# Optimization experiments

Hardware: AMD Instinct MI355X
Metric: run time of the kernel (lower is better)

Reference implementation:

```python
import jax, jax.numpy as jnp
import numpy as np
import math

D_MODEL = 1024
NUM_HEADS = 16
ROPE_THETA = 10000.0
BATCH = 4
SEQ = 2048


def apply_rope(x, pos, theta=ROPE_THETA):
    # x: (b, h, s, d_k), pos: (s,) int positions
    d = x.shape[-1]
    inv_freq = theta ** (-jnp.arange(0, d, 2, dtype=jnp.float32) / d)  # (d/2,)
    ang = pos.astype(jnp.float32)[:, None] * inv_freq                  # (s, d/2)
    cos, sin = jnp.cos(ang), jnp.sin(ang)
    x1, x2 = x[..., 0::2], x[..., 1::2]
    # interleave rotated pairs back to last dim
    out = jnp.stack([x1 * cos - x2 * sin, x1 * sin + x2 * cos], axis=-1)
    return out.reshape(x.shape)


def setup_inputs() -> dict:
    key = jax.random.key(0)
    ks = jax.random.split(key, 5)
    scale = 1.0 / math.sqrt(D_MODEL)
    return {
        "x": jax.random.normal(ks[0], (BATCH, SEQ, D_MODEL), dtype=jnp.float32),
        "token_positions": jnp.arange(SEQ, dtype=jnp.int64 if jax.config.jax_enable_x64 else jnp.int32),
        "Wq": jax.random.normal(ks[1], (D_MODEL, D_MODEL), dtype=jnp.float32) * scale,
        "Wk": jax.random.normal(ks[2], (D_MODEL, D_MODEL), dtype=jnp.float32) * scale,
        "Wv": jax.random.normal(ks[3], (D_MODEL, D_MODEL), dtype=jnp.float32) * scale,
        "Wo": jax.random.normal(ks[4], (D_MODEL, D_MODEL), dtype=jnp.float32) * scale,
    }


def reference(x, token_positions, Wq, Wk, Wv, Wo):
    b, s, d_model = x.shape
    h = NUM_HEADS
    d_k = d_model // h

    def proj_split(W):
        # Linear: y = x @ W.T (W is (out,in)); then split heads -> (b, h, s, d_k)
        y = jnp.einsum('bsi,oi->bso', x, W)
        return y.reshape(b, s, h, d_k).transpose(0, 2, 1, 3)

    q = apply_rope(proj_split(Wq), token_positions)
    k = apply_rope(proj_split(Wk), token_positions)
    v = proj_split(Wv)

    scores = jnp.einsum('bhqd,bhkd->bhqk', q, k) / jnp.asarray(math.sqrt(d_k), x.dtype)
    causal = jnp.tril(jnp.ones((s, s), dtype=bool))  # (s, s) keep lower triangle
    scores = jnp.where(causal, scores, jnp.asarray(-jnp.inf, scores.dtype))
    attn = jax.nn.softmax(scores, axis=-1)
    out = jnp.einsum('bhqk,bhkd->bhqd', attn, v)
    out = out.transpose(0, 2, 1, 3).reshape(b, s, d_model)
    return jnp.einsum('bsi,oi->bso', out, Wo)
```

## Files before the change

kernel.cpp:

```cpp
#include <hip/hip_runtime.h>
#include <cstdint>
#include <cstddef>


typedef __attribute__((ext_vector_type(8))) short bf16x8;
typedef __attribute__((ext_vector_type(4))) float f32x4;

#define LOG2E 1.4426950408889634f

__device__ __forceinline__ unsigned short f2bf(float f) {
  unsigned int u = __builtin_bit_cast(unsigned int, f);
  unsigned int r = (u + 0x7FFFu + ((u >> 16) & 1u)) >> 16;
  return (unsigned short)r;
}
__device__ __forceinline__ float bf2f(unsigned short h) {
  return __builtin_bit_cast(float, (unsigned int)h << 16);
}
__device__ __forceinline__ unsigned int packbf2(float a, float b) {
  return (unsigned int)f2bf(a) | ((unsigned int)f2bf(b) << 16);
}
__device__ __forceinline__ int swz(int idx) {
  return idx ^ (((idx >> 6) & 7) << 3);
}

__global__ __launch_bounds__(256) void cvt_kernel(const float* __restrict__ in,
                                                  unsigned short* __restrict__ out,
                                                  int n8) {
  int i = blockIdx.x * 256 + threadIdx.x;
  if (i < n8) {
    float4 u0 = ((const float4*)in)[i * 2];
    float4 u1 = ((const float4*)in)[i * 2 + 1];
    uint4 v = {packbf2(u0.x, u0.y), packbf2(u0.z, u0.w),
               packbf2(u1.x, u1.y), packbf2(u1.z, u1.w)};
    ((uint4*)out)[i] = v;
  }
}
__global__ __launch_bounds__(256) void cvt_w3(const float* __restrict__ w0,
                                              const float* __restrict__ w1,
                                              const float* __restrict__ w2,
                                              unsigned short* __restrict__ dst) {
  const float* src = blockIdx.y == 0 ? w0 : (blockIdx.y == 1 ? w1 : w2);
  unsigned short* d = dst + (size_t)blockIdx.y * 1024 * 1024;
  int i = blockIdx.x * 256 + threadIdx.x;
  float4 u0 = ((const float4*)src)[i * 2];
  float4 u1 = ((const float4*)src)[i * 2 + 1];
  uint4 v = {packbf2(u0.x, u0.y), packbf2(u0.z, u0.w),
             packbf2(u1.x, u1.y), packbf2(u1.z, u1.w)};
  ((uint4*)d)[i] = v;
}

__global__ __launch_bounds__(256) void gemm_qkv(const unsigned short* __restrict__ Xb,
                                                const unsigned short* __restrict__ Wb3,
                                                unsigned short* __restrict__ Qb,
                                                unsigned short* __restrict__ Kb,
                                                unsigned short* __restrict__ Vtb) {
  __shared__ alignas(16) unsigned short As[128 * 64];
  __shared__ alignas(16) unsigned short Bs[128 * 64];
  const int t = threadIdx.x;
  const int lane = t & 63;
  const int w = t >> 6;
  const int wr = w >> 1, wc = w & 1;
  const int fr = lane & 15, fq = lane >> 4;
  const int m0 = blockIdx.x * 128;
  const int sel = blockIdx.y >> 3;
  const int n0 = (blockIdx.y & 7) * 128;
  const unsigned short* Wp = Wb3 + (size_t)sel * 1024 * 1024;
  const int K = 1024;

  const f32x4 zero = {0.f, 0.f, 0.f, 0.f};
  f32x4 acc[4][4];
#pragma unroll
  for (int m = 0; m < 4; ++m)
#pragma unroll
    for (int n = 0; n < 4; ++n) acc[m][n] = zero;

  for (int k0 = 0; k0 < K; k0 += 64) {
#pragma unroll
    for (int cc = 0; cc < 4; ++cc) {
      int c = w * 4 + cc;
      int flat = c * 512 + lane * 8;
      int row = flat >> 6, col = flat & 63;
      __builtin_amdgcn_global_load_lds(
          (const __attribute__((address_space(1))) void*)(Xb + (size_t)(m0 + row) * K + (k0 + col)),
          (__attribute__((address_space(3))) void*)&As[c * 512], 16, 0, 0);
      __builtin_amdgcn_global_load_lds(
          (const __attribute__((address_space(1))) void*)(Wp + (size_t)(n0 + row) * K + (k0 + col)),
          (__attribute__((address_space(3))) void*)&Bs[c * 512], 16, 0, 0);
    }
    __syncthreads();
#pragma unroll
    for (int kk = 0; kk < 2; ++kk) {
      bf16x8 a[4], b[4];
#pragma unroll
      for (int m = 0; m < 4; ++m)
        a[m] = *(const bf16x8*)&As[(wr * 64 + m * 16 + fr) * 64 + kk * 32 + fq * 8];
#pragma unroll
      for (int n = 0; n < 4; ++n)
        b[n] = *(const bf16x8*)&Bs[(wc * 64 + n * 16 + fr) * 64 + kk * 32 + fq * 8];
#pragma unroll
      for (int m = 0; m < 4; ++m)
#pragma unroll
        for (int n = 0; n < 4; ++n)
          acc[m][n] = __builtin_amdgcn_mfma_f32_16x16x32_bf16(a[m], b[n], acc[m][n], 0, 0, 0);
    }
    __syncthreads();
  }

#pragma unroll
  for (int m = 0; m < 4; ++m)
#pragma unroll
    for (int n = 0; n < 4; ++n) {
      int row = m0 + wr * 64 + m * 16 + fq * 4;
      int col = n0 + wc * 64 + n * 16 + fr;
      if (sel < 2) {
        unsigned short* Cp = sel ? Kb : Qb;
#pragma unroll
        for (int j = 0; j < 4; ++j)
          Cp[(size_t)(row + j) * 1024 + col] = f2bf(acc[m][n][j]);
      } else {
        int b = row >> 11, s = row & 2047;
        int h = col >> 6, d = col & 63;
        ushort4 v4 = {f2bf(acc[m][n][0]), f2bf(acc[m][n][1]),
                      f2bf(acc[m][n][2]), f2bf(acc[m][n][3])};
        *(ushort4*)&Vtb[(((size_t)b * 16 + h) * 64 + d) * 2048 + s] = v4;
      }
    }
}

__global__ __launch_bounds__(256) void rope_kernel(unsigned short* __restrict__ Q,
                                                   unsigned short* __restrict__ Kb,
                                                   const int* __restrict__ tp) {
  int idx = blockIdx.x * 256 + threadIdx.x;
  unsigned short* ptr = blockIdx.y ? Kb : Q;
  const float scale = blockIdx.y ? 1.0f : 0.125f * LOG2E;
  int flat8 = idx * 8;
  int r = flat8 >> 10;
  int colbase = flat8 & 1023;
  int ibase = (colbase & 63) >> 1;
  int s = r & 2047;
  float pos = (float)tp[s];
  const float cexp = -13.287712379549449f / 32.0f;

  uint4 v = *(const uint4*)&ptr[flat8];
  unsigned int* vp = (unsigned int*)&v;
  uint4 o;
  unsigned int* op = (unsigned int*)&o;
#pragma unroll
  for (int p = 0; p < 4; ++p) {
    float inv = exp2f((float)(ibase + p) * cexp);
    float ang = pos * inv;
    float sn, cs;
    sincosf(ang, &sn, &cs);
    float x1 = bf2f((unsigned short)(vp[p] & 0xFFFFu));
    float x2 = bf2f((unsigned short)(vp[p] >> 16));
    op[p] = packbf2((x1 * cs - x2 * sn) * scale, (x1 * sn + x2 * cs) * scale);
  }
  *(uint4*)&ptr[flat8] = o;
}

__global__ __launch_bounds__(512, 2) void attn_kernel(const unsigned short* __restrict__ Q,
                                                      const unsigned short* __restrict__ K,
                                                      const unsigned short* __restrict__ Vt_g,
                                                      unsigned short* __restrict__ O) {
  __shared__ alignas(16) unsigned short Ks[64 * 64];
  __shared__ alignas(16) unsigned short Vt[64 * 64];
  const int t = threadIdx.x;
  const int lane = t & 63, w = t >> 6;
  const int fr = lane & 15, fq = lane >> 4;
  const int gblk = (blockIdx.x & 7) * 64 + (blockIdx.x >> 3);
  const int qt = gblk & 7;
  const int hb = gblk >> 3;
  const int h = hb & 15, b = hb >> 4;
  const int q0 = qt * 256;
  const size_t base = ((size_t)b * 2048) * 1024 + (size_t)h * 64;
  const size_t vbase = ((size_t)b * 16 + h) * 64 * 2048;
  const f32x4 zero = {0.f, 0.f, 0.f, 0.f};

  bf16x8 qf[2][2];
#pragma unroll
  for (int g = 0; g < 2; ++g)
#pragma unroll
    for (int kk = 0; kk < 2; ++kk)
      qf[g][kk] = *(const bf16x8*)&Q[base + (size_t)(q0 + w * 32 + g * 16 + fr) * 1024 + kk * 32 + fq * 8];

  float m_[2] = {-INFINITY, -INFINITY};
  float l_[2] = {0.f, 0.f};
  f32x4 oaccT[2][4];
#pragma unroll
  for (int g = 0; g < 2; ++g)
#pragma unroll
    for (int n = 0; n < 4; ++n) oaccT[g][n] = zero;

  const int sflat = t * 8;
  const int srow = sflat >> 6, scol = sflat & 63;
  const int sdst = swz(sflat);
  uint4 kr = *(const uint4*)&K[base + (size_t)srow * 1024 + scol];
  uint4 vr = *(const uint4*)&Vt_g[vbase + (size_t)srow * 2048 + scol];
  const int kvend = q0 + 256;
  const int wq = q0 + w * 32;

  for (int kv0 = 0; kv0 < kvend; kv0 += 64) {
    __syncthreads();
    *(uint4*)&Ks[sdst] = kr;
    *(uint4*)&Vt[sdst] = vr;
    __syncthreads();
    if (kv0 + 64 < kvend) {
      kr = *(const uint4*)&K[base + (size_t)(kv0 + 64 + srow) * 1024 + scol];
      vr = *(const uint4*)&Vt_g[vbase + (size_t)srow * 2048 + kv0 + 64 + scol];
    }

    if (kv0 <= wq + 31) {
      bf16x8 kf[2][4];
#pragma unroll
      for (int kk = 0; kk < 2; ++kk)
#pragma unroll
        for (int n = 0; n < 4; ++n)
          kf[kk][n] = *(const bf16x8*)&Ks[swz((n * 16 + fr) * 64 + kk * 32 + fq * 8)];

#pragma unroll
      for (int g = 0; g < 2; ++g) {
        if (kv0 > wq + g * 16 + 15) continue;
        f32x4 sa[4];
#pragma unroll
        for (int n = 0; n < 4; ++n) sa[n] = zero;
#pragma unroll
        for (int kk = 0; kk < 2; ++kk)
#pragma unroll
          for (int n = 0; n < 4; ++n)
            sa[n] = __builtin_amdgcn_mfma_f32_16x16x32_bf16(kf[kk][n], qf[g][kk], sa[n], 0, 0, 0);

        const int dd = kv0 - wq - g * 16;
        const bool diag = (dd > -63);
        float pmax = -3.0e38f;
#pragma unroll
        for (int n = 0; n < 4; ++n)
#pragma unroll
          for (int j = 0; j < 4; ++j) {
            float s = sa[n][j];
            if (diag && (n * 16 + fq * 4 + j + dd > fr)) s = -3.0e38f;
            sa[n][j] = s;
            pmax = fmaxf(pmax, s);
          }
        pmax = fmaxf(pmax, __shfl_xor(pmax, 16));
        pmax = fmaxf(pmax, __shfl_xor(pmax, 32));
        float mn = fmaxf(m_[g], pmax);
        float alpha = exp2f(m_[g] - mn);
        m_[g] = mn;
        float ps = 0.f;
#pragma unroll
        for (int n = 0; n < 4; ++n)
#pragma unroll
          for (int j = 0; j < 4; ++j) {
            float e = exp2f(sa[n][j] - mn);
            sa[n][j] = e;
            ps += e;
          }
        ps += __shfl_xor(ps, 16);
        ps += __shfl_xor(ps, 32);
        l_[g] = l_[g] * alpha + ps;
#pragma unroll
        for (int n = 0; n < 4; ++n)
#pragma unroll
          for (int j = 0; j < 4; ++j) oaccT[g][n][j] *= alpha;

        unsigned R[4][2], F[4][2];
#pragma unroll
        for (int n = 0; n < 4; ++n)
#pragma unroll
          for (int pp = 0; pp < 2; ++pp)
            R[n][pp] = packbf2(sa[n][2 * pp], sa[n][2 * pp + 1]);
#pragma unroll
        for (int pp = 0; pp < 2; ++pp) {
          unsigned t0 = (fq < 2) ? R[1][pp] : R[0][pp];
          unsigned t1 = (fq < 2) ? R[3][pp] : R[2][pp];
          t0 = (unsigned)__shfl_xor((int)t0, 32);
          t1 = (unsigned)__shfl_xor((int)t1, 32);
          unsigned G0 = (fq < 2) ? R[0][pp] : t0;
          unsigned G1 = (fq < 2) ? t0 : R[1][pp];
          unsigned G2 = (fq < 2) ? R[2][pp] : t1;
          unsigned G3 = (fq < 2) ? t1 : R[3][pp];
          unsigned u0 = ((fq & 1) == 0) ? G1 : G0;
          unsigned u1 = ((fq & 1) == 0) ? G3 : G2;
          u0 = (unsigned)__shfl_xor((int)u0, 16);
          u1 = (unsigned)__shfl_xor((int)u1, 16);
          F[0][pp] = ((fq & 1) == 0) ? G0 : u0;
          F[1][pp] = ((fq & 1) == 0) ? u0 : G1;
          F[2][pp] = ((fq & 1) == 0) ? G2 : u1;
          F[3][pp] = ((fq & 1) == 0) ? u1 : G3;
        }
        union U8 { unsigned u[4]; bf16x8 v; };
        U8 pb0, pb1;
        pb0.u[0] = F[0][0]; pb0.u[1] = F[0][1]; pb0.u[2] = F[1][0]; pb0.u[3] = F[1][1];
        pb1.u[0] = F[2][0]; pb1.u[1] = F[2][1]; pb1.u[2] = F[3][0]; pb1.u[3] = F[3][1];

#pragma unroll
        for (int n = 0; n < 4; ++n) {
          bf16x8 vf0 = *(const bf16x8*)&Vt[swz((n * 16 + fr) * 64 + 0 * 32 + fq * 8)];
          oaccT[g][n] = __builtin_amdgcn_mfma_f32_16x16x32_bf16(vf0, pb0.v, oaccT[g][n], 0, 0, 0);
          bf16x8 vf1 = *(const bf16x8*)&Vt[swz((n * 16 + fr) * 64 + 1 * 32 + fq * 8)];
          oaccT[g][n] = __builtin_amdgcn_mfma_f32_16x16x32_bf16(vf1, pb1.v, oaccT[g][n], 0, 0, 0);
        }
      }
    }
  }

#pragma unroll
  for (int g = 0; g < 2; ++g) {
    float rl = 1.0f / l_[g];
#pragma unroll
    for (int n = 0; n < 4; ++n) {
      ushort4 v4 = {f2bf(oaccT[g][n][0] * rl), f2bf(oaccT[g][n][1] * rl),
                    f2bf(oaccT[g][n][2] * rl), f2bf(oaccT[g][n][3] * rl)};
      *(ushort4*)&O[base + (size_t)(q0 + w * 32 + g * 16 + fr) * 1024 + n * 16 + fq * 4] = v4;
    }
  }
}

__global__ __launch_bounds__(256) void gemm_out_bf(const unsigned short* __restrict__ Ap,
                                                   const unsigned short* __restrict__ Wp,
                                                   float* __restrict__ Cp) {
  __shared__ alignas(16) unsigned short As[128 * 64];
  __shared__ alignas(16) unsigned short Bs[128 * 64];
  const int t = threadIdx.x;
  const int lane = t & 63;
  const int w = t >> 6;
  const int wr = w >> 1, wc = w & 1;
  const int fr = lane & 15, fq = lane >> 4;
  const int m0 = blockIdx.x * 128, n0 = blockIdx.y * 128;
  const int K = 1024, N = 1024;

  const f32x4 zero = {0.f, 0.f, 0.f, 0.f};
  f32x4 acc[4][4];
#pragma unroll
  for (int m = 0; m < 4; ++m)
#pragma unroll
    for (int n = 0; n < 4; ++n) acc[m][n] = zero;

  for (int k0 = 0; k0 < K; k0 += 64) {
#pragma unroll
    for (int cc = 0; cc < 4; ++cc) {
      int c = w * 4 + cc;
      int flat = c * 512 + lane * 8;
      int row = flat >> 6, col = flat & 63;
      __builtin_amdgcn_global_load_lds(
          (const __attribute__((address_space(1))) void*)(Ap + (size_t)(m0 + row) * K + (k0 + col)),
          (__attribute__((address_space(3))) void*)&As[c * 512], 16, 0, 0);
      __builtin_amdgcn_global_load_lds(
          (const __attribute__((address_space(1))) void*)(Wp + (size_t)(n0 + row) * K + (k0 + col)),
          (__attribute__((address_space(3))) void*)&Bs[c * 512], 16, 0, 0);
    }
    __syncthreads();
#pragma unroll
    for (int kk = 0; kk < 2; ++kk) {
      bf16x8 a[4], b[4];
#pragma unroll
      for (int m = 0; m < 4; ++m)
        a[m] = *(const bf16x8*)&As[(wr * 64 + m * 16 + fr) * 64 + kk * 32 + fq * 8];
#pragma unroll
      for (int n = 0; n < 4; ++n)
        b[n] = *(const bf16x8*)&Bs[(wc * 64 + n * 16 + fr) * 64 + kk * 32 + fq * 8];
#pragma unroll
      for (int m = 0; m < 4; ++m)
#pragma unroll
        for (int n = 0; n < 4; ++n)
          acc[m][n] = __builtin_amdgcn_mfma_f32_16x16x32_bf16(a[m], b[n], acc[m][n], 0, 0, 0);
    }
    __syncthreads();
  }

#pragma unroll
  for (int m = 0; m < 4; ++m)
#pragma unroll
    for (int n = 0; n < 4; ++n) {
      int row = m0 + wr * 64 + m * 16 + fq * 4;
      int col = n0 + wc * 64 + n * 16 + fr;
#pragma unroll
      for (int j = 0; j < 4; ++j)
        Cp[(size_t)(row + j) * N + col] = acc[m][n][j];
    }
}

extern "C" void kernel_launch(void* const* d_in, const int* in_sizes, int n_in,
                              void* d_out, int out_size, void* d_ws, size_t ws_size,
                              hipStream_t stream) {
  const float* x  = (const float*)d_in[0];
  const int* tp   = (const int*)d_in[1];
  const float* Wq = (const float*)d_in[2];
  const float* Wk = (const float*)d_in[3];
  const float* Wv = (const float*)d_in[4];
  const float* Wo = (const float*)d_in[5];
  float* out = (float*)d_out;

  const size_t MAT = (size_t)8192 * 1024;
  unsigned short* Qb  = (unsigned short*)d_ws;
  unsigned short* Kb  = Qb + MAT;
  unsigned short* Vtb = Kb + MAT;
  unsigned short* Xb  = Vtb + MAT;
  unsigned short* Ob  = Xb;
  unsigned short* Wb3 = (unsigned short*)d_out;
  unsigned short* WoB = Qb;

  cvt_kernel<<<4096, 256, 0, stream>>>(x, Xb, 8192 * 1024 / 8);
  cvt_w3<<<dim3(512, 3), 256, 0, stream>>>(Wq, Wk, Wv, Wb3);
  gemm_qkv<<<dim3(64, 24), 256, 0, stream>>>(Xb, Wb3, Qb, Kb, Vtb);
  rope_kernel<<<dim3(4096, 2), 256, 0, stream>>>(Qb, Kb, tp);
  attn_kernel<<<512, 512, 0, stream>>>(Qb, Kb, Vtb, Ob);
  cvt_kernel<<<512, 256, 0, stream>>>(Wo, WoB, 1024 * 1024 / 8);
  gemm_out_bf<<<dim3(64, 8), 256, 0, stream>>>(Ob, WoB, out);
}
```

Measured before the change: 413.4 us.

## Balance causal attention work by pairing light and heavy query tiles per block

```diff
diff --git a/kernel.cpp b/kernel.cpp
--- a/kernel.cpp
+++ b/kernel.cpp
@@ -158,160 +158,177 @@
   *(uint4*)&ptr[flat8] = o;
 }
 
-__global__ __launch_bounds__(512, 2) void attn_kernel(const unsigned short* __restrict__ Q,
-                                                      const unsigned short* __restrict__ K,
-                                                      const unsigned short* __restrict__ Vt_g,
-                                                      unsigned short* __restrict__ O) {
+__global__ __launch_bounds__(256) void attn_kernel(const unsigned short* __restrict__ Q,
+                                                   const unsigned short* __restrict__ K,
+                                                   const unsigned short* __restrict__ Vt_g,
+                                                   unsigned short* __restrict__ O) {
   __shared__ alignas(16) unsigned short Ks[64 * 64];
   __shared__ alignas(16) unsigned short Vt[64 * 64];
   const int t = threadIdx.x;
   const int lane = t & 63, w = t >> 6;
   const int fr = lane & 15, fq = lane >> 4;
   const int gblk = (blockIdx.x & 7) * 64 + (blockIdx.x >> 3);
-  const int qt = gblk & 7;
+  const int pairidx = gblk & 7;
   const int hb = gblk >> 3;
   const int h = hb & 15, b = hb >> 4;
-  const int q0 = qt * 256;
   const size_t base = ((size_t)b * 2048) * 1024 + (size_t)h * 64;
   const size_t vbase = ((size_t)b * 16 + h) * 64 * 2048;
   const f32x4 zero = {0.f, 0.f, 0.f, 0.f};
 
-  bf16x8 qf[2][2];
-#pragma unroll
-  for (int g = 0; g < 2; ++g)
-#pragma unroll
-    for (int kk = 0; kk < 2; ++kk)
-      qf[g][kk] = *(const bf16x8*)&Q[base + (size_t)(q0 + w * 32 + g * 16 + fr) * 1024 + kk * 32 + fq * 8];
-
-  float m_[2] = {-INFINITY, -INFINITY};
-  float l_[2] = {0.f, 0.f};
-  f32x4 oaccT[2][4];
-#pragma unroll
-  for (int g = 0; g < 2; ++g)
-#pragma unroll
-    for (int n = 0; n < 4; ++n) oaccT[g][n] = zero;
-
   const int sflat = t * 8;
-  const int srow = sflat >> 6, scol = sflat & 63;
-  const int sdst = swz(sflat);
-  uint4 kr = *(const uint4*)&K[base + (size_t)srow * 1024 + scol];
-  uint4 vr = *(const uint4*)&Vt_g[vbase + (size_t)srow * 2048 + scol];
-  const int kvend = q0 + 256;
-  const int wq = q0 + w * 32;
-
-  for (int kv0 = 0; kv0 < kvend; kv0 += 64) {
-    __syncthreads();
-    *(uint4*)&Ks[sdst] = kr;
-    *(uint4*)&Vt[sdst] = vr;
-    __syncthreads();
-    if (kv0 + 64 < kvend) {
-      kr = *(const uint4*)&K[base + (size_t)(kv0 + 64 + srow) * 1024 + scol];
-      vr = *(const uint4*)&Vt_g[vbase + (size_t)srow * 2048 + kv0 + 64 + scol];
-    }
-
-    if (kv0 <= wq + 31) {
-      bf16x8 kf[2][4];
+  const int srow0 = sflat >> 6, scol = sflat & 63;
+
+  for (int pass = 0; pass < 2; ++pass) {
+    const int qt = pass ? (15 - pairidx) : pairidx;
+    const int q0 = qt * 128;
+    const int wq = q0 + w * 32;
+    const int kvend = q0 + 128;
+
+    bf16x8 qf[2][2];
+#pragma unroll
+    for (int g = 0; g < 2; ++g)
 #pragma unroll
       for (int kk = 0; kk < 2; ++kk)
-#pragma unroll
-        for (int n = 0; n < 4; ++n)
-          kf[kk][n] = *(const bf16x8*)&Ks[swz((n * 16 + fr) * 64 + kk * 32 + fq * 8)];
-
-#pragma unroll
-      for (int g = 0; g < 2; ++g) {
-        if (kv0 > wq + g * 16 + 15) continue;
-        f32x4 sa[4];
-#pragma unroll
-        for (int n = 0; n < 4; ++n) sa[n] = zero;
-#pragma unroll
-        for (int kk = 0; kk < 2; ++kk)
-#pragma unroll
-          for (int n = 0; n < 4; ++n)
-            sa[n] = __builtin_amdgcn_mfma_f32_16x16x32_bf16(kf[kk][n], qf[g][kk], sa[n], 0, 0, 0);
-
-        const int dd = kv0 - wq - g * 16;
-        const bool diag = (dd > -63);
-        float pmax = -3.0e38f;
-#pragma unroll
-        for (int n = 0; n < 4; ++n)
-#pragma unroll
-          for (int j = 0; j < 4; ++j) {
-            float s = sa[n][j];
-            if (diag && (n * 16 + fq * 4 + j + dd > fr)) s = -3.0e38f;
-            sa[n][j] = s;
-            pmax = fmaxf(pmax, s);
-          }
-        pmax = fmaxf(pmax, __shfl_xor(pmax, 16));
-        pmax = fmaxf(pmax, __shfl_xor(pmax, 32));
-        float mn = fmaxf(m_[g], pmax);
-        float alpha = exp2f(m_[g] - mn);
-        m_[g] = mn;
-        float ps = 0.f;
-#pragma unroll
-        for (int n = 0; n < 4; ++n)
-#pragma unroll
-          for (int j = 0; j < 4; ++j) {
-            float e = exp2f(sa[n][j] - mn);
-            sa[n][j] = e;
-            ps += e;
-          }
-        ps += __shfl_xor(ps, 16);
-        ps += __shfl_xor(ps, 32);
-        l_[g] = l_[g] * alpha + ps;
-#pragma unroll
-        for (int n = 0; n < 4; ++n)
-#pragma unroll
-          for (int j = 0; j < 4; ++j) oaccT[g][n][j] *= alpha;
-
-        unsigned R[4][2], F[4][2];
-#pragma unroll
-        for (int n = 0; n < 4; ++n)
-#pragma unroll
-          for (int pp = 0; pp < 2; ++pp)
-            R[n][pp] = packbf2(sa[n][2 * pp], sa[n][2 * pp + 1]);
-#pragma unroll
-        for (int pp = 0; pp < 2; ++pp) {
-          unsigned t0 = (fq < 2) ? R[1][pp] : R[0][pp];
-          unsigned t1 = (fq < 2) ? R[3][pp] : R[2][pp];
-          t0 = (unsigned)__shfl_xor((int)t0, 32);
-          t1 = (unsigned)__shfl_xor((int)t1, 32);
-          unsigned G0 = (fq < 2) ? R[0][pp] : t0;
-          unsigned G1 = (fq < 2) ? t0 : R[1][pp];
-          unsigned G2 = (fq < 2) ? R[2][pp] : t1;
-          unsigned G3 = (fq < 2) ? t1 : R[3][pp];
-          unsigned u0 = ((fq & 1) == 0) ? G1 : G0;
-          unsigned u1 = ((fq & 1) == 0) ? G3 : G2;
-          u0 = (unsigned)__shfl_xor((int)u0, 16);
-          u1 = (unsigned)__shfl_xor((int)u1, 16);
-          F[0][pp] = ((fq & 1) == 0) ? G0 : u0;
-          F[1][pp] = ((fq & 1) == 0) ? u0 : G1;
-          F[2][pp] = ((fq & 1) == 0) ? G2 : u1;
-          F[3][pp] = ((fq & 1) == 0) ? u1 : G3;
-        }
-        union U8 { unsigned u[4]; bf16x8 v; };
-        U8 pb0, pb1;
-        pb0.u[0] = F[0][0]; pb0.u[1] = F[0][1]; pb0.u[2] = F[1][0]; pb0.u[3] = F[1][1];
-        pb1.u[0] = F[2][0]; pb1.u[1] = F[2][1]; pb1.u[2] = F[3][0]; pb1.u[3] = F[3][1];
-
-#pragma unroll
-        for (int n = 0; n < 4; ++n) {
-          bf16x8 vf0 = *(const bf16x8*)&Vt[swz((n * 16 + fr) * 64 + 0 * 32 + fq * 8)];
-          oaccT[g][n] = __builtin_amdgcn_mfma_f32_16x16x32_bf16(vf0, pb0.v, oaccT[g][n], 0, 0, 0);
-          bf16x8 vf1 = *(const bf16x8*)&Vt[swz((n * 16 + fr) * 64 + 1 * 32 + fq * 8)];
-          oaccT[g][n] = __builtin_amdgcn_mfma_f32_16x16x32_bf16(vf1, pb1.v, oaccT[g][n], 0, 0, 0);
+        qf[g][kk] = *(const bf16x8*)&Q[base + (size_t)(q0 + w * 32 + g * 16 + fr) * 1024 + kk * 32 + fq * 8];
+
+    float m_[2] = {-INFINITY, -INFINITY};
+    float l_[2] = {0.f, 0.f};
+    f32x4 oaccT[2][4];
+#pragma unroll
+    for (int g = 0; g < 2; ++g)
+#pragma unroll
+      for (int n = 0; n < 4; ++n) oaccT[g][n] = zero;
+
+    uint4 kr[2], vr[2];
+#pragma unroll
+    for (int it = 0; it < 2; ++it) {
+      int row = srow0 + it * 32;
+      kr[it] = *(const uint4*)&K[base + (size_t)row * 1024 + scol];
+      vr[it] = *(const uint4*)&Vt_g[vbase + (size_t)row * 2048 + scol];
+    }
+
+    for (int kv0 = 0; kv0 < kvend; kv0 += 64) {
+      __syncthreads();
+#pragma unroll
+      for (int it = 0; it < 2; ++it) {
+        int flat = sflat + it * 2048;
+        *(uint4*)&Ks[swz(flat)] = kr[it];
+        *(uint4*)&Vt[swz(flat)] = vr[it];
+      }
+      __syncthreads();
+      if (kv0 + 64 < kvend) {
+#pragma unroll
+        for (int it = 0; it < 2; ++it) {
+          int row = srow0 + it * 32;
+          kr[it] = *(const uint4*)&K[base + (size_t)(kv0 + 64 + row) * 1024 + scol];
+          vr[it] = *(const uint4*)&Vt_g[vbase + (size_t)row * 2048 + kv0 + 64 + scol];
         }
       }
-    }
-  }
-
-#pragma unroll
-  for (int g = 0; g < 2; ++g) {
-    float rl = 1.0f / l_[g];
-#pragma unroll
-    for (int n = 0; n < 4; ++n) {
-      ushort4 v4 = {f2bf(oaccT[g][n][0] * rl), f2bf(oaccT[g][n][1] * rl),
-                    f2bf(oaccT[g][n][2] * rl), f2bf(oaccT[g][n][3] * rl)};
-      *(ushort4*)&O[base + (size_t)(q0 + w * 32 + g * 16 + fr) * 1024 + n * 16 + fq * 4] = v4;
+
+      if (kv0 <= wq + 31) {
+        bf16x8 kf[2][4];
+#pragma unroll
+        for (int kk = 0; kk < 2; ++kk)
+#pragma unroll
+          for (int n = 0; n < 4; ++n)
+            kf[kk][n] = *(const bf16x8*)&Ks[swz((n * 16 + fr) * 64 + kk * 32 + fq * 8)];
+
+#pragma unroll
+        for (int g = 0; g < 2; ++g) {
+          if (kv0 > wq + g * 16 + 15) continue;
+          f32x4 sa[4];
+#pragma unroll
+          for (int n = 0; n < 4; ++n) sa[n] = zero;
+#pragma unroll
+          for (int kk = 0; kk < 2; ++kk)
+#pragma unroll
+            for (int n = 0; n < 4; ++n)
+              sa[n] = __builtin_amdgcn_mfma_f32_16x16x32_bf16(kf[kk][n], qf[g][kk], sa[n], 0, 0, 0);
+
+          const int dd = kv0 - wq - g * 16;
+          const bool diag = (dd > -63);
+          float pmax = -3.0e38f;
+#pragma unroll
+          for (int n = 0; n < 4; ++n)
+#pragma unroll
+            for (int j = 0; j < 4; ++j) {
+              float s = sa[n][j];
+              if (diag && (n * 16 + fq * 4 + j + dd > fr)) s = -3.0e38f;
+              sa[n][j] = s;
+              pmax = fmaxf(pmax, s);
+            }
+          pmax = fmaxf(pmax, __shfl_xor(pmax, 16));
+          pmax = fmaxf(pmax, __shfl_xor(pmax, 32));
+          float mn = fmaxf(m_[g], pmax);
+          float alpha = exp2f(m_[g] - mn);
+          m_[g] = mn;
+          float ps = 0.f;
+#pragma unroll
+          for (int n = 0; n < 4; ++n)
+#pragma unroll
+            for (int j = 0; j < 4; ++j) {
+              float e = exp2f(sa[n][j] - mn);
+              sa[n][j] = e;
+              ps += e;
+            }
+          ps += __shfl_xor(ps, 16);
+          ps += __shfl_xor(ps, 32);
+          l_[g] = l_[g] * alpha + ps;
+#pragma unroll
+          for (int n = 0; n < 4; ++n)
+#pragma unroll
+            for (int j = 0; j < 4; ++j) oaccT[g][n][j] *= alpha;
+
+          unsigned R[4][2], F[4][2];
+#pragma unroll
+          for (int n = 0; n < 4; ++n)
+#pragma unroll
+            for (int pp = 0; pp < 2; ++pp)
+              R[n][pp] = packbf2(sa[n][2 * pp], sa[n][2 * pp + 1]);
+#pragma unroll
+          for (int pp = 0; pp < 2; ++pp) {
+            unsigned t0 = (fq < 2) ? R[1][pp] : R[0][pp];
+            unsigned t1 = (fq < 2) ? R[3][pp] : R[2][pp];
+            t0 = (unsigned)__shfl_xor((int)t0, 32);
+            t1 = (unsigned)__shfl_xor((int)t1, 32);
+            unsigned G0 = (fq < 2) ? R[0][pp] : t0;
+            unsigned G1 = (fq < 2) ? t0 : R[1][pp];
+            unsigned G2 = (fq < 2) ? R[2][pp] : t1;
+            unsigned G3 = (fq < 2) ? t1 : R[3][pp];
+            unsigned u0 = ((fq & 1) == 0) ? G1 : G0;
+            unsigned u1 = ((fq & 1) == 0) ? G3 : G2;
+            u0 = (unsigned)__shfl_xor((int)u0, 16);
+            u1 = (unsigned)__shfl_xor((int)u1, 16);
+            F[0][pp] = ((fq & 1) == 0) ? G0 : u0;
+            F[1][pp] = ((fq & 1) == 0) ? u0 : G1;
+            F[2][pp] = ((fq & 1) == 0) ? G2 : u1;
+            F[3][pp] = ((fq & 1) == 0) ? u1 : G3;
+          }
+          union U8 { unsigned u[4]; bf16x8 v; };
+          U8 pb0, pb1;
+          pb0.u[0] = F[0][0]; pb0.u[1] = F[0][1]; pb0.u[2] = F[1][0]; pb0.u[3] = F[1][1];
+          pb1.u[0] = F[2][0]; pb1.u[1] = F[2][1]; pb1.u[2] = F[3][0]; pb1.u[3] = F[3][1];
+
+#pragma unroll
+          for (int n = 0; n < 4; ++n) {
+            bf16x8 vf0 = *(const bf16x8*)&Vt[swz((n * 16 + fr) * 64 + 0 * 32 + fq * 8)];
+            oaccT[g][n] = __builtin_amdgcn_mfma_f32_16x16x32_bf16(vf0, pb0.v, oaccT[g][n], 0, 0, 0);
+            bf16x8 vf1 = *(const bf16x8*)&Vt[swz((n * 16 + fr) * 64 + 1 * 32 + fq * 8)];
+            oaccT[g][n] = __builtin_amdgcn_mfma_f32_16x16x32_bf16(vf1, pb1.v, oaccT[g][n], 0, 0, 0);
+          }
+        }
+      }
+    }
+
+#pragma unroll
+    for (int g = 0; g < 2; ++g) {
+      float rl = 1.0f / l_[g];
+#pragma unroll
+      for (int n = 0; n < 4; ++n) {
+        ushort4 v4 = {f2bf(oaccT[g][n][0] * rl), f2bf(oaccT[g][n][1] * rl),
+                      f2bf(oaccT[g][n][2] * rl), f2bf(oaccT[g][n][3] * rl)};
+        *(ushort4*)&O[base + (size_t)(q0 + w * 32 + g * 16 + fr) * 1024 + n * 16 + fq * 4] = v4;
+      }
     }
   }
 }
@@ -404,7 +421,7 @@
   cvt_w3<<<dim3(512, 3), 256, 0, stream>>>(Wq, Wk, Wv, Wb3);
   gemm_qkv<<<dim3(64, 24), 256, 0, stream>>>(Xb, Wb3, Qb, Kb, Vtb);
   rope_kernel<<<dim3(4096, 2), 256, 0, stream>>>(Qb, Kb, tp);
-  attn_kernel<<<512, 512, 0, stream>>>(Qb, Kb, Vtb, Ob);
+  attn_kernel<<<512, 256, 0, stream>>>(Qb, Kb, Vtb, Ob);
   cvt_kernel<<<512, 256, 0, stream>>>(Wo, WoB, 1024 * 1024 / 8);
   gemm_out_bf<<<dim3(64, 8), 256, 0, stream>>>(Ob, WoB, out);
 }
```

Result: faster. 364.2 us (-11.9%).
